# Kernel tuning notes

Measured on AMD Instinct MI355X. Metric: run time of the kernel, lower is better.

## Reference

```python
import jax, jax.numpy as jnp
import numpy as np

N_NODES = 200000
N_EDGES = 3200000
N_GRAPHS = 64
IN_DIM, HIDDEN, OUT_DIM = 128, 16, 64


def setup_inputs() -> dict:
    key = jax.random.key(0)
    ks = jax.random.split(key, 5)
    x = jax.random.normal(ks[0], (N_NODES, IN_DIM), dtype=jnp.float32)
    edge_index = jax.random.randint(ks[1], (2, N_EDGES), 0, N_NODES, dtype=jnp.int64)
    batch = jnp.sort(jax.random.randint(ks[2], (N_NODES,), 0, N_GRAPHS, dtype=jnp.int64))
    W1 = jax.random.normal(ks[3], (IN_DIM, HIDDEN), dtype=jnp.float32) * (1.0 / np.sqrt(IN_DIM))
    W2 = jax.random.normal(ks[4], (HIDDEN, OUT_DIM), dtype=jnp.float32) * (1.0 / np.sqrt(HIDDEN))
    b1 = jnp.zeros((HIDDEN,), jnp.float32)
    b2 = jnp.zeros((OUT_DIM,), jnp.float32)
    return {"x": x, "edge_index": edge_index, "batch": batch,
            "W1": W1, "b1": b1, "W2": W2, "b2": b2, "training": 0}


def _gcn_conv(x, W, b, row, col, n_nodes):
    # PyG GCNConv: add-self-loop symmetric normalization, transform then
    # gather-from-row / scatter-add-to-col.  (row, col) already include self-loops.
    h = x @ W                                             # [N, out]
    deg = jnp.zeros((n_nodes,), h.dtype).at[col].add(1.0)  # degree incl. self-loop (>=1)
    dinv = deg ** -0.5
    norm = dinv[row] * dinv[col]                          # [E+N]
    out = jnp.zeros((n_nodes, W.shape[1]), h.dtype).at[col].add(h[row] * norm[:, None])
    return out + b


def reference(x, edge_index, batch, W1, b1, W2, b2, training):
    n = x.shape[0]
    loops = jnp.arange(n, dtype=edge_index.dtype)
    row = jnp.concatenate([edge_index[0], loops])
    col = jnp.concatenate([edge_index[1], loops])
    h = _gcn_conv(x, W1, b1, row, col, n)
    h = jax.nn.relu(h)
    # F.dropout with training=False is identity (reference is deterministic)
    h = _gcn_conv(h, W2, b2, row, col, n)
    # per-graph sum pooling: replaces the Python torch.where loop
    graph_embeds = jax.ops.segment_sum(h, batch, num_segments=N_GRAPHS)
    return graph_embeds
```

## Files before the change

### kernel.cpp

```cpp
#include <hip/hip_runtime.h>


#define TPB 256
#define CHUNK 4096
#define BK_SHIFT 9
#define NPB 512

__device__ __forceinline__ float bf2f(unsigned short u) {
    union { unsigned int i; float f; } v; v.i = ((unsigned int)u) << 16; return v.f;
}
__device__ __forceinline__ unsigned short f2bf(float f) {
    union { float f; unsigned int i; } v; v.f = f;
    unsigned int r = v.i + 0x7fff + ((v.i >> 16) & 1);
    return (unsigned short)(r >> 16);
}

__global__ __launch_bounds__(TPB) void hist_kernel(const int* __restrict__ col,
                                                   int* __restrict__ counts,
                                                   int E, int nblk, int nbuck) {
    __shared__ int hist[512];
    int t = threadIdx.x;
    for (int i = t; i < nbuck; i += TPB) hist[i] = 0;
    __syncthreads();
    int e0 = blockIdx.x * CHUNK;
    for (int i = t; i < CHUNK; i += TPB) {
        int e = e0 + i;
        if (e < E) atomicAdd(&hist[col[e] >> BK_SHIFT], 1);
    }
    __syncthreads();
    for (int i = t; i < nbuck; i += TPB) counts[i * nblk + blockIdx.x] = hist[i];
}

__global__ __launch_bounds__(TPB) void scan1_kernel(const int* __restrict__ in,
                                                    int* __restrict__ out,
                                                    int* __restrict__ bsum, int L) {
    __shared__ int s[TPB];
    int t = threadIdx.x;
    int i = blockIdx.x * TPB + t;
    int d = (i < L) ? in[i] : 0;
    s[t] = d; __syncthreads();
    for (int off = 1; off < TPB; off <<= 1) {
        int v = (t >= off) ? s[t - off] : 0;
        __syncthreads();
        s[t] += v;
        __syncthreads();
    }
    if (i < L) out[i] = s[t] - d;
    if (t == TPB - 1) bsum[blockIdx.x] = s[t];
}

__global__ __launch_bounds__(1024) void scan2_kernel(int* __restrict__ bsum, int nb) {
    __shared__ int s[1024];
    int t = threadIdx.x;
    int i0 = t * 2, i1 = t * 2 + 1;
    int v0 = (i0 < nb) ? bsum[i0] : 0;
    int v1 = (i1 < nb) ? bsum[i1] : 0;
    int pv = v0 + v1;
    s[t] = pv; __syncthreads();
    for (int off = 1; off < 1024; off <<= 1) {
        int u = (t >= off) ? s[t - off] : 0;
        __syncthreads();
        s[t] += u;
        __syncthreads();
    }
    int exc = s[t] - pv;
    if (i0 < nb) bsum[i0] = exc;
    if (i1 < nb) bsum[i1] = exc + v0;
}

__global__ __launch_bounds__(TPB) void scan3g_kernel(int* __restrict__ out,
                                                     const int* __restrict__ bsum, int L) {
    int i = blockIdx.x * TPB + threadIdx.x;
    if (i < L) out[i] += bsum[blockIdx.x];
}

__global__ __launch_bounds__(TPB) void s1c_gemm_kernel(
        const int* __restrict__ row, const int* __restrict__ col,
        const int* __restrict__ cbase, int E, int nblk, int nbuck,
        int* __restrict__ bucketed,
        const float* __restrict__ x, const float* __restrict__ W1,
        float* __restrict__ h1, int N, int nbg) {
    __shared__ int cur[NPB];
    __shared__ float w1s[128 * 16];
    int b = (int)blockIdx.x, t = threadIdx.x;
    int M = min(nblk, nbg);
    int role, id;
    if (b < 2 * M) { role = b & 1; id = b >> 1; }
    else           { role = (nblk > nbg) ? 0 : 1; id = b - M; }

    if (role == 0) {
        for (int i = t; i < nbuck; i += TPB) cur[i] = cbase[i * nblk + id];
        __syncthreads();
        int e0 = id * CHUNK;
        for (int i = t; i < CHUNK; i += TPB) {
            int e = e0 + i;
            if (e < E) {
                int c = col[e];
                int pos = atomicAdd(&cur[c >> BK_SHIFT], 1);
                bucketed[pos] = ((c & (NPB - 1)) << 18) | row[e];
            }
        }
        return;
    }
    for (int i = t; i < 128 * 16; i += TPB) w1s[i] = W1[i];
    __syncthreads();
    int n = id * TPB + t;
    if (n >= N) return;
    const float4* xr = (const float4*)(x + (size_t)n * 128);
    float acc[16];
#pragma unroll
    for (int k = 0; k < 16; ++k) acc[k] = 0.f;
#pragma unroll 1
    for (int g = 0; g < 8; ++g) {
        float4 v0 = xr[g * 4 + 0], v1 = xr[g * 4 + 1];
        float4 v2 = xr[g * 4 + 2], v3 = xr[g * 4 + 3];
        float xv[16] = {v0.x, v0.y, v0.z, v0.w, v1.x, v1.y, v1.z, v1.w,
                        v2.x, v2.y, v2.z, v2.w, v3.x, v3.y, v3.z, v3.w};
#pragma unroll
        for (int cc = 0; cc < 16; ++cc) {
            const float4* w4 = (const float4*)&w1s[(g * 16 + cc) * 16];
            float4 wa = w4[0], wb = w4[1], wc = w4[2], wd = w4[3];
            float xc = xv[cc];
            acc[0]  = fmaf(xc, wa.x, acc[0]);  acc[1]  = fmaf(xc, wa.y, acc[1]);
            acc[2]  = fmaf(xc, wa.z, acc[2]);  acc[3]  = fmaf(xc, wa.w, acc[3]);
            acc[4]  = fmaf(xc, wb.x, acc[4]);  acc[5]  = fmaf(xc, wb.y, acc[5]);
            acc[6]  = fmaf(xc, wb.z, acc[6]);  acc[7]  = fmaf(xc, wb.w, acc[7]);
            acc[8]  = fmaf(xc, wc.x, acc[8]);  acc[9]  = fmaf(xc, wc.y, acc[9]);
            acc[10] = fmaf(xc, wc.z, acc[10]); acc[11] = fmaf(xc, wc.w, acc[11]);
            acc[12] = fmaf(xc, wd.x, acc[12]); acc[13] = fmaf(xc, wd.y, acc[13]);
            acc[14] = fmaf(xc, wd.z, acc[14]); acc[15] = fmaf(xc, wd.w, acc[15]);
        }
    }
    float4* o = (float4*)(h1 + (size_t)n * 16);
    o[0] = make_float4(acc[0], acc[1], acc[2], acc[3]);
    o[1] = make_float4(acc[4], acc[5], acc[6], acc[7]);
    o[2] = make_float4(acc[8], acc[9], acc[10], acc[11]);
    o[3] = make_float4(acc[12], acc[13], acc[14], acc[15]);
}

__global__ __launch_bounds__(TPB) void sort_kernel(
        const int* __restrict__ bucketed, const int* __restrict__ cbase,
        int E, int nblk, int nbuck,
        int* __restrict__ csr, int* __restrict__ offs, float* __restrict__ dinv,
        const float* __restrict__ h1, unsigned short* __restrict__ h1p, int N) {
    __shared__ int lhist[NPB];
    __shared__ int part[TPB];
    __shared__ float sdinv[NPB];
    int bk = blockIdx.x, t = threadIdx.x;
    int n0 = bk << BK_SHIFT;
    int n1 = min(n0 + NPB, N);
    int e0 = cbase[bk * nblk];
    int e1 = (bk + 1 < nbuck) ? cbase[(bk + 1) * nblk] : E;

    lhist[t] = 0; lhist[t + TPB] = 0;
    __syncthreads();
    for (int i = e0 + t; i < e1; i += TPB)
        atomicAdd(&lhist[bucketed[i] >> 18], 1);
    __syncthreads();

    int base = t * 2;
    int c0 = lhist[base], c1 = lhist[base + 1];
    int s = c0 + c1;
    part[t] = s;
    __syncthreads();
    for (int off = 1; off < TPB; off <<= 1) {
        int v = (t >= off) ? part[t - off] : 0;
        __syncthreads();
        part[t] += v;
        __syncthreads();
    }
    int o0 = e0 + part[t] - s;
    int o1 = o0 + c0;
    lhist[base] = o0; lhist[base + 1] = o1;
    sdinv[base]     = rsqrtf((float)c0 + 1.0f);
    sdinv[base + 1] = rsqrtf((float)c1 + 1.0f);
    int n = n0 + base;
    if (n + 0 < N) { offs[n + 0] = o0; dinv[n + 0] = sdinv[base]; }
    if (n + 1 < N) { offs[n + 1] = o1; dinv[n + 1] = sdinv[base + 1]; }
    __syncthreads();

    for (int i = e0 + t; i < e1; i += TPB) {
        int v = bucketed[i];
        int pos = atomicAdd(&lhist[v >> 18], 1);
        csr[pos] = v & 0x3FFFF;
    }
    int nq = (n1 - n0) * 4;
    for (int i = t; i < nq; i += TPB) {
        float dv = sdinv[i >> 2];
        float4 v = ((const float4*)h1)[(size_t)n0 * 4 + i];
        ((ushort4*)h1p)[(size_t)n0 * 4 + i] =
            make_ushort4(f2bf(v.x * dv), f2bf(v.y * dv), f2bf(v.z * dv), f2bf(v.w * dv));
    }
    if (bk == 0 && t == 0) offs[N] = E;
}

__global__ __launch_bounds__(TPB) void gather1_kernel(const int* __restrict__ csr,
                                                      const int* __restrict__ offs,
                                                      const unsigned short* __restrict__ h1p,
                                                      const float* __restrict__ dinv,
                                                      const float* __restrict__ b1,
                                                      unsigned short* __restrict__ h2p, int N) {
    int t = threadIdx.x;
    int c = blockIdx.x * 16 + (t >> 4);
    int k = t & 15;
    if (c >= N) return;
    int p0 = offs[c], p1 = offs[c + 1];
    float acc = 0.f;
    for (int p = p0; p < p1; p += 32) {
        int s0 = csr[min(p + k, p1 - 1)];
        int s1 = csr[min(p + 16 + k, p1 - 1)];
        int rem = p1 - p;
        float v[32];
#pragma unroll
        for (int j = 0; j < 16; ++j) {
            int sj = __shfl(s0, j, 16);
            v[j] = bf2f(h1p[(size_t)sj * 16 + k]);
        }
#pragma unroll
        for (int j = 0; j < 16; ++j) {
            int sj = __shfl(s1, j, 16);
            v[16 + j] = bf2f(h1p[(size_t)sj * 16 + k]);
        }
#pragma unroll
        for (int j = 0; j < 32; ++j) acc += (j < rem) ? v[j] : 0.f;
    }
    float dc = dinv[c];
    float self = bf2f(h1p[(size_t)c * 16 + k]);
    float a = fmaf(dc, acc + self, b1[k]);
    h2p[(size_t)c * 16 + k] = f2bf(dc * fmaxf(a, 0.f));
}

__global__ __launch_bounds__(TPB) void gather2_kernel(const int* __restrict__ csr,
                                                      const int* __restrict__ offs,
                                                      const unsigned short* __restrict__ h2p,
                                                      const float* __restrict__ dinv,
                                                      float* __restrict__ a2, int N) {
    int t = threadIdx.x;
    int c = blockIdx.x * 16 + (t >> 4);
    int k = t & 15;
    if (c >= N) return;
    int p0 = offs[c], p1 = offs[c + 1];
    float acc = 0.f;
    for (int p = p0; p < p1; p += 32) {
        int s0 = csr[min(p + k, p1 - 1)];
        int s1 = csr[min(p + 16 + k, p1 - 1)];
        int rem = p1 - p;
        float v[32];
#pragma unroll
        for (int j = 0; j < 16; ++j) {
            int sj = __shfl(s0, j, 16);
            v[j] = bf2f(h2p[(size_t)sj * 16 + k]);
        }
#pragma unroll
        for (int j = 0; j < 16; ++j) {
            int sj = __shfl(s1, j, 16);
            v[16 + j] = bf2f(h2p[(size_t)sj * 16 + k]);
        }
#pragma unroll
        for (int j = 0; j < 32; ++j) acc += (j < rem) ? v[j] : 0.f;
    }
    float self = bf2f(h2p[(size_t)c * 16 + k]);
    a2[(size_t)c * 16 + k] = dinv[c] * (acc + self);
}

__global__ __launch_bounds__(TPB) void final_kernel(const float* __restrict__ a2,
                                                    const float* __restrict__ W2,
                                                    const float* __restrict__ b2,
                                                    const int* __restrict__ batch,
                                                    float* __restrict__ out, int N) {
    __shared__ float w2s[16 * 64];
    int t = threadIdx.x;
    for (int i = t; i < 16 * 64; i += TPB) w2s[i] = W2[i];
    __syncthreads();

    int wave = t >> 6, lane = t & 63;
    int n0 = blockIdx.x * 256 + wave * 64;
    float b2k = b2[lane];
    int g_cur = -1;
    float acc = 0.f;
    for (int i = 0; i < 64; ++i) {
        int n = n0 + i;
        if (n >= N) break;
        const float* ar = a2 + (size_t)n * 16;
        float val = b2k;
#pragma unroll
        for (int j = 0; j < 16; ++j) val = fmaf(ar[j], w2s[j * 64 + lane], val);
        int g = batch[n];
        if (g != g_cur) {
            if (g_cur >= 0) atomicAdd(&out[(size_t)g_cur * 64 + lane], acc);
            acc = 0.f;
            g_cur = g;
        }
        acc += val;
    }
    if (g_cur >= 0) atomicAdd(&out[(size_t)g_cur * 64 + lane], acc);
}

static inline size_t align64(size_t v) { return (v + 63) & ~(size_t)63; }

extern "C" void kernel_launch(void* const* d_in, const int* in_sizes, int n_in,
                              void* d_out, int out_size, void* d_ws, size_t ws_size,
                              hipStream_t stream) {
    const float* x     = (const float*)d_in[0];
    const int*   ei    = (const int*)d_in[1];
    const int*   batch = (const int*)d_in[2];
    const float* W1    = (const float*)d_in[3];
    const float* b1    = (const float*)d_in[4];
    const float* W2    = (const float*)d_in[5];
    const float* b2    = (const float*)d_in[6];

    const int N = in_sizes[0] / 128;
    const int E = in_sizes[1] / 2;
    const int* row = ei;
    const int* col = ei + E;

    const int NBLK  = (E + CHUNK - 1) / CHUNK;
    const int NBUCK = (N + NPB - 1) / NPB;
    const int L     = NBUCK * NBLK;
    const int NBS   = (L + TPB - 1) / TPB;
    const int NBG   = (N + TPB - 1) / TPB;

    char* p = (char*)d_ws;
    int*            counts   = (int*)p;            p += align64((size_t)L * 4);
    int*            bsum     = (int*)p;            p += align64(2048 * 4);
    int*            bucketed = (int*)p;            p += align64((size_t)E * 4);
    int*            csr      = (int*)p;            p += align64((size_t)E * 4);
    int*            offs     = (int*)p;            p += align64((size_t)(N + 1) * 4);
    float*          dinv     = (float*)p;          p += align64((size_t)N * 4);
    float*          h1       = (float*)p;          p += align64((size_t)N * 16 * 4);
    unsigned short* h1p      = (unsigned short*)p; p += align64((size_t)N * 16 * 2);
    unsigned short* h2p      = (unsigned short*)p; p += align64((size_t)N * 16 * 2);
    float*          a2       = h1;
    float*          out      = (float*)d_out;

    hipMemsetAsync(out, 0, (size_t)out_size * sizeof(float), stream);

    hist_kernel<<<NBLK, TPB, 0, stream>>>(col, counts, E, NBLK, NBUCK);
    scan1_kernel<<<NBS, TPB, 0, stream>>>(counts, counts, bsum, L);
    scan2_kernel<<<1, 1024, 0, stream>>>(bsum, NBS);
    scan3g_kernel<<<NBS, TPB, 0, stream>>>(counts, bsum, L);
    s1c_gemm_kernel<<<NBLK + NBG, TPB, 0, stream>>>(row, col, counts, E, NBLK, NBUCK,
                                                    bucketed, x, W1, h1, N, NBG);
    sort_kernel<<<NBUCK, TPB, 0, stream>>>(bucketed, counts, E, NBLK, NBUCK,
                                           csr, offs, dinv, h1, h1p, N);
    gather1_kernel<<<(N + 15) / 16, TPB, 0, stream>>>(csr, offs, h1p, dinv, b1, h2p, N);
    gather2_kernel<<<(N + 15) / 16, TPB, 0, stream>>>(csr, offs, h2p, dinv, a2, N);
    final_kernel<<<(N + 255) / 256, TPB, 0, stream>>>(a2, W2, b2, batch, out, N);
}
```

Baseline: 374.5 us.

## Fuse gather2 with final projection/pooling, drop scan3 pass, store h1 as bf16

Three changes. The scan3 add-pass is removed, and consumers now compute bucket bases on the fly as counts plus the block sum. The first-layer GEMM writes h1 in bf16 instead of fp32, which halves that intermediate's write and read traffic at some added rounding. The second gather is fused with the W2 projection and per-graph pooling: results go through LDS instead of an fp32 a2 buffer, and blocks whose 64 nodes all belong to one graph reduce in shared memory before issuing the global atomics.

```diff
diff --git a/kernel.cpp b/kernel.cpp
--- a/kernel.cpp
+++ b/kernel.cpp
@@ -68,18 +68,17 @@
     if (i1 < nb) bsum[i1] = exc + v0;
 }
 
-__global__ __launch_bounds__(TPB) void scan3g_kernel(int* __restrict__ out,
-                                                     const int* __restrict__ bsum, int L) {
-    int i = blockIdx.x * TPB + threadIdx.x;
-    if (i < L) out[i] += bsum[blockIdx.x];
+__device__ __forceinline__ int cbase_at(const int* counts, const int* bsum, int f) {
+    return counts[f] + bsum[f >> 8];
 }
 
 __global__ __launch_bounds__(TPB) void s1c_gemm_kernel(
         const int* __restrict__ row, const int* __restrict__ col,
-        const int* __restrict__ cbase, int E, int nblk, int nbuck,
+        const int* __restrict__ counts, const int* __restrict__ bsum,
+        int E, int nblk, int nbuck,
         int* __restrict__ bucketed,
         const float* __restrict__ x, const float* __restrict__ W1,
-        float* __restrict__ h1, int N, int nbg) {
+        unsigned short* __restrict__ h1b, int N, int nbg) {
     __shared__ int cur[NPB];
     __shared__ float w1s[128 * 16];
     int b = (int)blockIdx.x, t = threadIdx.x;
@@ -89,7 +88,8 @@
     else           { role = (nblk > nbg) ? 0 : 1; id = b - M; }
 
     if (role == 0) {
-        for (int i = t; i < nbuck; i += TPB) cur[i] = cbase[i * nblk + id];
+        for (int i = t; i < nbuck; i += TPB)
+            cur[i] = cbase_at(counts, bsum, i * nblk + id);
         __syncthreads();
         int e0 = id * CHUNK;
         for (int i = t; i < CHUNK; i += TPB) {
@@ -131,26 +131,29 @@
             acc[14] = fmaf(xc, wd.z, acc[14]); acc[15] = fmaf(xc, wd.w, acc[15]);
         }
     }
-    float4* o = (float4*)(h1 + (size_t)n * 16);
-    o[0] = make_float4(acc[0], acc[1], acc[2], acc[3]);
-    o[1] = make_float4(acc[4], acc[5], acc[6], acc[7]);
-    o[2] = make_float4(acc[8], acc[9], acc[10], acc[11]);
-    o[3] = make_float4(acc[12], acc[13], acc[14], acc[15]);
+    unsigned int u[8];
+#pragma unroll
+    for (int j = 0; j < 8; ++j)
+        u[j] = (unsigned int)f2bf(acc[2 * j]) | ((unsigned int)f2bf(acc[2 * j + 1]) << 16);
+    uint4* o = (uint4*)(h1b + (size_t)n * 16);
+    o[0] = make_uint4(u[0], u[1], u[2], u[3]);
+    o[1] = make_uint4(u[4], u[5], u[6], u[7]);
 }
 
 __global__ __launch_bounds__(TPB) void sort_kernel(
-        const int* __restrict__ bucketed, const int* __restrict__ cbase,
+        const int* __restrict__ bucketed,
+        const int* __restrict__ counts, const int* __restrict__ bsum,
         int E, int nblk, int nbuck,
         int* __restrict__ csr, int* __restrict__ offs, float* __restrict__ dinv,
-        const float* __restrict__ h1, unsigned short* __restrict__ h1p, int N) {
+        const unsigned short* __restrict__ h1b, unsigned short* __restrict__ h1p, int N) {
     __shared__ int lhist[NPB];
     __shared__ int part[TPB];
     __shared__ float sdinv[NPB];
     int bk = blockIdx.x, t = threadIdx.x;
     int n0 = bk << BK_SHIFT;
     int n1 = min(n0 + NPB, N);
-    int e0 = cbase[bk * nblk];
-    int e1 = (bk + 1 < nbuck) ? cbase[(bk + 1) * nblk] : E;
+    int e0 = cbase_at(counts, bsum, bk * nblk);
+    int e1 = (bk + 1 < nbuck) ? cbase_at(counts, bsum, (bk + 1) * nblk) : E;
 
     lhist[t] = 0; lhist[t + TPB] = 0;
     __syncthreads();
@@ -187,9 +190,13 @@
     int nq = (n1 - n0) * 4;
     for (int i = t; i < nq; i += TPB) {
         float dv = sdinv[i >> 2];
-        float4 v = ((const float4*)h1)[(size_t)n0 * 4 + i];
+        uint2 u = ((const uint2*)h1b)[(size_t)n0 * 4 + i];
+        float f0 = bf2f((unsigned short)(u.x & 0xffff));
+        float f1 = bf2f((unsigned short)(u.x >> 16));
+        float f2 = bf2f((unsigned short)(u.y & 0xffff));
+        float f3 = bf2f((unsigned short)(u.y >> 16));
         ((ushort4*)h1p)[(size_t)n0 * 4 + i] =
-            make_ushort4(f2bf(v.x * dv), f2bf(v.y * dv), f2bf(v.z * dv), f2bf(v.w * dv));
+            make_ushort4(f2bf(f0 * dv), f2bf(f1 * dv), f2bf(f2 * dv), f2bf(f3 * dv));
     }
     if (bk == 0 && t == 0) offs[N] = E;
 }
@@ -230,70 +237,90 @@
     h2p[(size_t)c * 16 + k] = f2bf(dc * fmaxf(a, 0.f));
 }
 
-__global__ __launch_bounds__(TPB) void gather2_kernel(const int* __restrict__ csr,
-                                                      const int* __restrict__ offs,
-                                                      const unsigned short* __restrict__ h2p,
-                                                      const float* __restrict__ dinv,
-                                                      float* __restrict__ a2, int N) {
-    int t = threadIdx.x;
-    int c = blockIdx.x * 16 + (t >> 4);
-    int k = t & 15;
-    if (c >= N) return;
-    int p0 = offs[c], p1 = offs[c + 1];
-    float acc = 0.f;
-    for (int p = p0; p < p1; p += 32) {
-        int s0 = csr[min(p + k, p1 - 1)];
-        int s1 = csr[min(p + 16 + k, p1 - 1)];
-        int rem = p1 - p;
-        float v[32];
-#pragma unroll
-        for (int j = 0; j < 16; ++j) {
-            int sj = __shfl(s0, j, 16);
-            v[j] = bf2f(h2p[(size_t)sj * 16 + k]);
-        }
-#pragma unroll
-        for (int j = 0; j < 16; ++j) {
-            int sj = __shfl(s1, j, 16);
-            v[16 + j] = bf2f(h2p[(size_t)sj * 16 + k]);
-        }
-#pragma unroll
-        for (int j = 0; j < 32; ++j) acc += (j < rem) ? v[j] : 0.f;
-    }
-    float self = bf2f(h2p[(size_t)c * 16 + k]);
-    a2[(size_t)c * 16 + k] = dinv[c] * (acc + self);
-}
-
-__global__ __launch_bounds__(TPB) void final_kernel(const float* __restrict__ a2,
-                                                    const float* __restrict__ W2,
-                                                    const float* __restrict__ b2,
-                                                    const int* __restrict__ batch,
-                                                    float* __restrict__ out, int N) {
+__global__ __launch_bounds__(TPB) void gather2f_kernel(
+        const int* __restrict__ csr, const int* __restrict__ offs,
+        const unsigned short* __restrict__ h2p, const float* __restrict__ dinv,
+        const float* __restrict__ W2, const float* __restrict__ b2,
+        const int* __restrict__ batch, float* __restrict__ out, int N) {
     __shared__ float w2s[16 * 64];
+    __shared__ float asT[64 * 17];
+    __shared__ float pool[64];
     int t = threadIdx.x;
     for (int i = t; i < 16 * 64; i += TPB) w2s[i] = W2[i];
-    __syncthreads();
-
-    int wave = t >> 6, lane = t & 63;
-    int n0 = blockIdx.x * 256 + wave * 64;
-    float b2k = b2[lane];
+    if (t < 64) pool[t] = 0.f;
+
+    int n0 = blockIdx.x * 64;
+    int nLast = min(n0 + 63, N - 1);
+    int g0 = batch[n0];
+    bool uniform = (batch[nLast] == g0);
+
+    int grp = t >> 4, k = t & 15;
+#pragma unroll 1
+    for (int it = 0; it < 4; ++it) {
+        int m = grp * 4 + it;
+        int c = n0 + m;
+        if (c < N) {
+            int p0 = offs[c], p1 = offs[c + 1];
+            float acc = 0.f;
+            for (int p = p0; p < p1; p += 32) {
+                int s0 = csr[min(p + k, p1 - 1)];
+                int s1 = csr[min(p + 16 + k, p1 - 1)];
+                int rem = p1 - p;
+                float v[32];
+#pragma unroll
+                for (int j = 0; j < 16; ++j) {
+                    int sj = __shfl(s0, j, 16);
+                    v[j] = bf2f(h2p[(size_t)sj * 16 + k]);
+                }
+#pragma unroll
+                for (int j = 0; j < 16; ++j) {
+                    int sj = __shfl(s1, j, 16);
+                    v[16 + j] = bf2f(h2p[(size_t)sj * 16 + k]);
+                }
+#pragma unroll
+                for (int j = 0; j < 32; ++j) acc += (j < rem) ? v[j] : 0.f;
+            }
+            float self = bf2f(h2p[(size_t)c * 16 + k]);
+            asT[m * 17 + k] = dinv[c] * (acc + self);
+        }
+    }
+    __syncthreads();
+
+    int wave = t >> 6, j = t & 63;
+    float w2reg[16];
+#pragma unroll
+    for (int kk = 0; kk < 16; ++kk) w2reg[kk] = w2s[kk * 64 + j];
+    float b2j = b2[j];
+    float val = 0.f;
     int g_cur = -1;
-    float acc = 0.f;
-    for (int i = 0; i < 64; ++i) {
-        int n = n0 + i;
-        if (n >= N) break;
-        const float* ar = a2 + (size_t)n * 16;
-        float val = b2k;
-#pragma unroll
-        for (int j = 0; j < 16; ++j) val = fmaf(ar[j], w2s[j * 64 + lane], val);
-        int g = batch[n];
-        if (g != g_cur) {
-            if (g_cur >= 0) atomicAdd(&out[(size_t)g_cur * 64 + lane], acc);
-            acc = 0.f;
-            g_cur = g;
-        }
-        acc += val;
-    }
-    if (g_cur >= 0) atomicAdd(&out[(size_t)g_cur * 64 + lane], acc);
+#pragma unroll 1
+    for (int mi = 0; mi < 16; ++mi) {
+        int m = wave * 16 + mi;
+        int c = n0 + m;
+        if (c >= N) break;
+        const float* ar = &asT[m * 17];
+        float y = b2j;
+#pragma unroll
+        for (int kk = 0; kk < 16; ++kk) y = fmaf(ar[kk], w2reg[kk], y);
+        if (uniform) {
+            val += y;
+        } else {
+            int g = batch[c];
+            if (g != g_cur) {
+                if (g_cur >= 0) atomicAdd(&out[(size_t)g_cur * 64 + j], val);
+                val = 0.f;
+                g_cur = g;
+            }
+            val += y;
+        }
+    }
+    if (uniform) {
+        atomicAdd(&pool[j], val);
+        __syncthreads();
+        if (t < 64) atomicAdd(&out[(size_t)g0 * 64 + t], pool[t]);
+    } else {
+        if (g_cur >= 0) atomicAdd(&out[(size_t)g_cur * 64 + j], val);
+    }
 }
 
 static inline size_t align64(size_t v) { return (v + 63) & ~(size_t)63; }
@@ -327,10 +354,9 @@
     int*            csr      = (int*)p;            p += align64((size_t)E * 4);
     int*            offs     = (int*)p;            p += align64((size_t)(N + 1) * 4);
     float*          dinv     = (float*)p;          p += align64((size_t)N * 4);
-    float*          h1       = (float*)p;          p += align64((size_t)N * 16 * 4);
+    unsigned short* h1b      = (unsigned short*)p; p += align64((size_t)N * 16 * 2);
     unsigned short* h1p      = (unsigned short*)p; p += align64((size_t)N * 16 * 2);
     unsigned short* h2p      = (unsigned short*)p; p += align64((size_t)N * 16 * 2);
-    float*          a2       = h1;
     float*          out      = (float*)d_out;
 
     hipMemsetAsync(out, 0, (size_t)out_size * sizeof(float), stream);
@@ -338,12 +364,12 @@
     hist_kernel<<<NBLK, TPB, 0, stream>>>(col, counts, E, NBLK, NBUCK);
     scan1_kernel<<<NBS, TPB, 0, stream>>>(counts, counts, bsum, L);
     scan2_kernel<<<1, 1024, 0, stream>>>(bsum, NBS);
-    scan3g_kernel<<<NBS, TPB, 0, stream>>>(counts, bsum, L);
-    s1c_gemm_kernel<<<NBLK + NBG, TPB, 0, stream>>>(row, col, counts, E, NBLK, NBUCK,
-                                                    bucketed, x, W1, h1, N, NBG);
-    sort_kernel<<<NBUCK, TPB, 0, stream>>>(bucketed, counts, E, NBLK, NBUCK,
-                                           csr, offs, dinv, h1, h1p, N);
+    s1c_gemm_kernel<<<NBLK + NBG, TPB, 0, stream>>>(row, col, counts, bsum,
+                                                    E, NBLK, NBUCK,
+                                                    bucketed, x, W1, h1b, N, NBG);
+    sort_kernel<<<NBUCK, TPB, 0, stream>>>(bucketed, counts, bsum, E, NBLK, NBUCK,
+                                           csr, offs, dinv, h1b, h1p, N);
     gather1_kernel<<<(N + 15) / 16, TPB, 0, stream>>>(csr, offs, h1p, dinv, b1, h2p, N);
-    gather2_kernel<<<(N + 15) / 16, TPB, 0, stream>>>(csr, offs, h2p, dinv, a2, N);
-    final_kernel<<<(N + 255) / 256, TPB, 0, stream>>>(a2, W2, b2, batch, out, N);
-}
+    gather2f_kernel<<<(N + 63) / 64, TPB, 0, stream>>>(csr, offs, h2p, dinv,
+                                                       W2, b2, batch, out, N);
+}
```

Measured after the change: 359.0 us. 4.2% less time.
